# Optimization experiments

Hardware: AMD Instinct MI355X
Metric: run time of the kernel (lower is better)

The kernel has to match this reference:

```python
import jax, jax.numpy as jnp
import numpy as np


def setup_inputs() -> dict:
    key = jax.random.key(0)
    k1, k2, k3, k4, k5 = jax.random.split(key, 5)
    D, K, W, C = 2048, 4096, 4096, 1000
    deep_feats = jax.random.normal(k1, (1, D), dtype=jnp.float32)
    cls_score = jax.random.normal(k2, (K, C), dtype=jnp.float32)
    target = jax.random.randint(k3, (1,), 0, C, dtype=jnp.int64)
    n = jax.random.normal(k4, (K, D), dtype=jnp.float32)
    w = jax.random.uniform(k5, (W, K), dtype=jnp.float32)
    return {"deep_feats": deep_feats, "cls_score": cls_score, "target": target, "n": n, "w": w}


def reference(deep_feats, cls_score, target, n, w):
    # d[idx] = ||deep_feats[0] - n[idx]||_2, shape [K]
    diff = deep_feats[0][None, :] - n            # [K, D]
    d = jnp.sqrt(jnp.sum(diff * diff, axis=-1))  # [K]
    # rho[idy] = softmax_idx(-w[idy] * d), shape [W, K]
    rho = jax.nn.softmax(-w * d[None, :], axis=-1)
    # f_loss = sum_{idy,idx} w[idy,idx] * d[idx]
    f_loss = jnp.sum(w * d[None, :])
    # per-neighbor cross entropy: ce[idx] = -log_softmax(cls_score[idx])[target]
    logp = jax.nn.log_softmax(cls_score, axis=-1)  # [K, C]
    ce = -logp[:, target[0]]                        # [K]
    # g_loss = sum_{idy,idx} rho[idy,idx] * ce[idx]
    g_loss = jnp.sum(rho @ ce)
    return g_loss + f_loss
```

## Files before the change

### kernel.cpp

```cpp
#include <hip/hip_runtime.h>
#include <math.h>

constexpr int KN = 4096;
constexpr int DN = 2048;
constexpr int CN = 1000;
constexpr int WN = 4096;

__device__ __forceinline__ float waveSum(float v) {
#pragma unroll
    for (int o = 32; o > 0; o >>= 1) v += __shfl_xor(v, o, 64);
    return v;
}
__device__ __forceinline__ float waveMax(float v) {
#pragma unroll
    for (int o = 32; o > 0; o >>= 1) v = fmaxf(v, __shfl_xor(v, o, 64));
    return v;
}

constexpr int S1_DIST_BLOCKS = KN / 4;
constexpr int S1_CE_BLOCKS   = KN / 4;

__global__ __launch_bounds__(256) void stage1_kernel(
    const float* __restrict__ deep, const float* __restrict__ nmat,
    const float* __restrict__ cls, const int* __restrict__ target,
    float* __restrict__ d_arr, float* __restrict__ ce_arr,
    float* __restrict__ out)
{
    const int b    = blockIdx.x;
    const int tid  = threadIdx.x;
    const int wv   = tid >> 6;
    const int lane = tid & 63;

    if (b == 0 && tid == 0)
        __hip_atomic_store(out, 0.0f, __ATOMIC_RELAXED, __HIP_MEMORY_SCOPE_AGENT);

    if (b < S1_DIST_BLOCKS) {
        const int row = b * 4 + wv;
        const float4* nrow = (const float4*)(nmat + (size_t)row * DN);
        const float4* df   = (const float4*)deep;
        float acc = 0.f;
#pragma unroll
        for (int c = 0; c < 8; ++c) {
            const int i = lane + 64 * c;
            const float4 a = df[i];
            const float4 x = nrow[i];
            const float e0 = a.x - x.x, e1 = a.y - x.y, e2 = a.z - x.z, e3 = a.w - x.w;
            acc += e0 * e0 + e1 * e1 + e2 * e2 + e3 * e3;
        }
        acc = waveSum(acc);
        if (lane == 0) d_arr[row] = sqrtf(acc);
    } else {
        const int row = (b - S1_DIST_BLOCKS) * 4 + wv;
        const float4* x4 = (const float4*)(cls + (size_t)row * CN);
        float4 v[4];
#pragma unroll
        for (int j = 0; j < 4; ++j) {
            const int i = lane + 64 * j;
            v[j] = (i < CN / 4) ? x4[i]
                                : make_float4(-INFINITY, -INFINITY, -INFINITY, -INFINITY);
        }
        float mx = -INFINITY;
#pragma unroll
        for (int j = 0; j < 4; ++j)
            mx = fmaxf(mx, fmaxf(fmaxf(v[j].x, v[j].y), fmaxf(v[j].z, v[j].w)));
        const float m = waveMax(mx);
        float s = 0.f;
#pragma unroll
        for (int j = 0; j < 4; ++j)
            s += __expf(v[j].x - m) + __expf(v[j].y - m)
               + __expf(v[j].z - m) + __expf(v[j].w - m);
        s = waveSum(s);
        if (lane == 0)
            ce_arr[row] = m + __logf(s) - cls[(size_t)row * CN + target[0]];
    }
}

constexpr int S2_BLOCK_THREADS = 512;
constexpr int S2_ROWS_PER_BLK  = 8;
constexpr int S2_BLOCKS        = WN / S2_ROWS_PER_BLK;

__global__ __launch_bounds__(S2_BLOCK_THREADS) void stage2_kernel(
    const float* __restrict__ wmat, const float* __restrict__ d_arr,
    const float* __restrict__ ce_arr, float* __restrict__ out)
{
    __shared__ float4 sd[KN / 4];
    __shared__ float4 sc[KN / 4];
    __shared__ float  part[8];

    const int tid  = threadIdx.x;
    const int wv   = tid >> 6;
    const int lane = tid & 63;

    {
        const float4* d4 = (const float4*)d_arr;
        const float4* c4 = (const float4*)ce_arr;
#pragma unroll
        for (int j = 0; j < 2; ++j) {
            const int i = tid + S2_BLOCK_THREADS * j;
            sd[i] = d4[i];
            sc[i] = c4[i];
        }
    }
    __syncthreads();

    const int row = blockIdx.x * S2_ROWS_PER_BLK + wv;
    const float4* wrow = (const float4*)(wmat + (size_t)row * KN);

    float es = 0.f, ec = 0.f, fs = 0.f;
#pragma unroll
    for (int c = 0; c < 16; ++c) {
        const int i = lane + 64 * c;
        const float4 a  = wrow[i];
        const float4 dv = sd[i];
        const float4 cv = sc[i];
        float t, e;
        t = a.x * dv.x; fs += t; e = __expf(-t); es += e; ec += e * cv.x;
        t = a.y * dv.y; fs += t; e = __expf(-t); es += e; ec += e * cv.y;
        t = a.z * dv.z; fs += t; e = __expf(-t); es += e; ec += e * cv.z;
        t = a.w * dv.w; fs += t; e = __expf(-t); es += e; ec += e * cv.w;
    }
    es = waveSum(es);  ec = waveSum(ec);  fs = waveSum(fs);

    if (lane == 0) part[wv] = ec / es + fs;
    __syncthreads();
    if (tid == 0) {
        float acc = 0.f;
#pragma unroll
        for (int j = 0; j < 8; ++j) acc += part[j];
        atomicAdd(out, acc);
    }
}

extern "C" void kernel_launch(void* const* d_in, const int* in_sizes, int n_in,
                              void* d_out, int out_size, void* d_ws, size_t ws_size,
                              hipStream_t stream) {
    const float* deep   = (const float*)d_in[0];
    const float* cls    = (const float*)d_in[1];
    const int*   target = (const int*)d_in[2];
    const float* nmat   = (const float*)d_in[3];
    const float* wmat   = (const float*)d_in[4];

    float* ws     = (float*)d_ws;
    float* d_arr  = ws;
    float* ce_arr = ws + KN;
    float* out    = (float*)d_out;

    stage1_kernel<<<S1_DIST_BLOCKS + S1_CE_BLOCKS, 256, 0, stream>>>(
        deep, nmat, cls, target, d_arr, ce_arr, out);
    stage2_kernel<<<S2_BLOCKS, S2_BLOCK_THREADS, 0, stream>>>(
        wmat, d_arr, ce_arr, out);
}
```

Before: 29.50 us.

## Fuse both stages into one persistent kernel with a global grid barrier

Merges the distance/cross-entropy stage and the weighted softmax stage into a single kernel of 1024 blocks. Each block does one distance row and one CE row per wave, then waits at an atomic-counter grid barrier before computing four w rows. A last-block reduction writes the output deterministically instead of using atomicAdd. This removes one kernel launch boundary, but adds a memset, a spin barrier that relies on every block being co-resident, and each block now loads the full d/ce vectors into LDS.

After: 79.28 us. 2.69x slower.

```diff
diff --git a/kernel.cpp b/kernel.cpp
--- a/kernel.cpp
+++ b/kernel.cpp
@@ -5,6 +5,9 @@
 constexpr int DN = 2048;
 constexpr int CN = 1000;
 constexpr int WN = 4096;
+
+constexpr int NBLK = 1024;
+constexpr int NTHR = 256;
 
 __device__ __forceinline__ float waveSum(float v) {
 #pragma unroll
@@ -17,25 +20,26 @@
     return v;
 }
 
-constexpr int S1_DIST_BLOCKS = KN / 4;
-constexpr int S1_CE_BLOCKS   = KN / 4;
-
-__global__ __launch_bounds__(256) void stage1_kernel(
+__global__ __launch_bounds__(NTHR, 4) void fused_kernel(
     const float* __restrict__ deep, const float* __restrict__ nmat,
     const float* __restrict__ cls, const int* __restrict__ target,
+    const float* __restrict__ wmat,
     float* __restrict__ d_arr, float* __restrict__ ce_arr,
+    float* __restrict__ part, unsigned int* __restrict__ cnt,
     float* __restrict__ out)
 {
+    __shared__ float sd[KN];
+    __shared__ float sc[KN];
+    __shared__ float wpart[4];
+    __shared__ int   sLast;
+
     const int b    = blockIdx.x;
     const int tid  = threadIdx.x;
     const int wv   = tid >> 6;
     const int lane = tid & 63;
+    const int row  = b * 4 + wv;
 
-    if (b == 0 && tid == 0)
-        __hip_atomic_store(out, 0.0f, __ATOMIC_RELAXED, __HIP_MEMORY_SCOPE_AGENT);
-
-    if (b < S1_DIST_BLOCKS) {
-        const int row = b * 4 + wv;
+    {
         const float4* nrow = (const float4*)(nmat + (size_t)row * DN);
         const float4* df   = (const float4*)deep;
         float acc = 0.f;
@@ -48,9 +52,12 @@
             acc += e0 * e0 + e1 * e1 + e2 * e2 + e3 * e3;
         }
         acc = waveSum(acc);
-        if (lane == 0) d_arr[row] = sqrtf(acc);
-    } else {
-        const int row = (b - S1_DIST_BLOCKS) * 4 + wv;
+        if (lane == 0)
+            __hip_atomic_store(&d_arr[row], sqrtf(acc),
+                               __ATOMIC_RELAXED, __HIP_MEMORY_SCOPE_AGENT);
+    }
+
+    {
         const float4* x4 = (const float4*)(cls + (size_t)row * CN);
         float4 v[4];
 #pragma unroll
@@ -71,63 +78,71 @@
                + __expf(v[j].z - m) + __expf(v[j].w - m);
         s = waveSum(s);
         if (lane == 0)
-            ce_arr[row] = m + __logf(s) - cls[(size_t)row * CN + target[0]];
+            ce_arr[row] = 0.f,
+            __hip_atomic_store(&ce_arr[row], m + __logf(s) - cls[(size_t)row * CN + target[0]],
+                               __ATOMIC_RELAXED, __HIP_MEMORY_SCOPE_AGENT);
     }
-}
 
-constexpr int S2_BLOCK_THREADS = 512;
-constexpr int S2_ROWS_PER_BLK  = 8;
-constexpr int S2_BLOCKS        = WN / S2_ROWS_PER_BLK;
+    asm volatile("s_waitcnt vmcnt(0)");
+    __syncthreads();
 
-__global__ __launch_bounds__(S2_BLOCK_THREADS) void stage2_kernel(
-    const float* __restrict__ wmat, const float* __restrict__ d_arr,
-    const float* __restrict__ ce_arr, float* __restrict__ out)
-{
-    __shared__ float4 sd[KN / 4];
-    __shared__ float4 sc[KN / 4];
-    __shared__ float  part[8];
-
-    const int tid  = threadIdx.x;
-    const int wv   = tid >> 6;
-    const int lane = tid & 63;
-
-    {
-        const float4* d4 = (const float4*)d_arr;
-        const float4* c4 = (const float4*)ce_arr;
-#pragma unroll
-        for (int j = 0; j < 2; ++j) {
-            const int i = tid + S2_BLOCK_THREADS * j;
-            sd[i] = d4[i];
-            sc[i] = c4[i];
-        }
+    if (tid == 0) {
+        __hip_atomic_fetch_add(cnt, 1u, __ATOMIC_RELAXED, __HIP_MEMORY_SCOPE_AGENT);
+        while (__hip_atomic_load(cnt, __ATOMIC_RELAXED, __HIP_MEMORY_SCOPE_AGENT)
+               < (unsigned)NBLK)
+            __builtin_amdgcn_s_sleep(8);
     }
     __syncthreads();
 
-    const int row = blockIdx.x * S2_ROWS_PER_BLK + wv;
-    const float4* wrow = (const float4*)(wmat + (size_t)row * KN);
+#pragma unroll
+    for (int j = 0; j < 16; ++j) {
+        const int i = tid + NTHR * j;
+        sd[i] = __hip_atomic_load(&d_arr[i],  __ATOMIC_RELAXED, __HIP_MEMORY_SCOPE_AGENT);
+        sc[i] = __hip_atomic_load(&ce_arr[i], __ATOMIC_RELAXED, __HIP_MEMORY_SCOPE_AGENT);
+    }
+    __syncthreads();
 
-    float es = 0.f, ec = 0.f, fs = 0.f;
+    {
+        const float4* wrow = (const float4*)(wmat + (size_t)row * KN);
+        const float4* sd4  = (const float4*)sd;
+        const float4* sc4  = (const float4*)sc;
+        float es = 0.f, ec = 0.f, fs = 0.f;
 #pragma unroll
-    for (int c = 0; c < 16; ++c) {
-        const int i = lane + 64 * c;
-        const float4 a  = wrow[i];
-        const float4 dv = sd[i];
-        const float4 cv = sc[i];
-        float t, e;
-        t = a.x * dv.x; fs += t; e = __expf(-t); es += e; ec += e * cv.x;
-        t = a.y * dv.y; fs += t; e = __expf(-t); es += e; ec += e * cv.y;
-        t = a.z * dv.z; fs += t; e = __expf(-t); es += e; ec += e * cv.z;
-        t = a.w * dv.w; fs += t; e = __expf(-t); es += e; ec += e * cv.w;
+        for (int c = 0; c < 16; ++c) {
+            const int i = lane + 64 * c;
+            const float4 a  = wrow[i];
+            const float4 dv = sd4[i];
+            const float4 cv = sc4[i];
+            float t, e;
+            t = a.x * dv.x; fs += t; e = __expf(-t); es += e; ec += e * cv.x;
+            t = a.y * dv.y; fs += t; e = __expf(-t); es += e; ec += e * cv.y;
+            t = a.z * dv.z; fs += t; e = __expf(-t); es += e; ec += e * cv.z;
+            t = a.w * dv.w; fs += t; e = __expf(-t); es += e; ec += e * cv.w;
+        }
+        es = waveSum(es);  ec = waveSum(ec);  fs = waveSum(fs);
+        if (lane == 0) wpart[wv] = ec / es + fs;
     }
-    es = waveSum(es);  ec = waveSum(ec);  fs = waveSum(fs);
+    __syncthreads();
 
-    if (lane == 0) part[wv] = ec / es + fs;
+    if (tid == 0) {
+        const float psum = wpart[0] + wpart[1] + wpart[2] + wpart[3];
+        __hip_atomic_store(&part[b], psum, __ATOMIC_RELAXED, __HIP_MEMORY_SCOPE_AGENT);
+        asm volatile("s_waitcnt vmcnt(0)");
+        const unsigned prev = __hip_atomic_fetch_add(cnt + 1, 1u, __ATOMIC_RELAXED,
+                                                     __HIP_MEMORY_SCOPE_AGENT);
+        sLast = (prev == (unsigned)(NBLK - 1)) ? 1 : 0;
+    }
     __syncthreads();
-    if (tid == 0) {
+    if (sLast) {
         float acc = 0.f;
 #pragma unroll
-        for (int j = 0; j < 8; ++j) acc += part[j];
-        atomicAdd(out, acc);
+        for (int j = 0; j < 4; ++j)
+            acc += __hip_atomic_load(&part[tid + NTHR * j],
+                                     __ATOMIC_RELAXED, __HIP_MEMORY_SCOPE_AGENT);
+        acc = waveSum(acc);
+        if (lane == 0) wpart[wv] = acc;
+        __syncthreads();
+        if (tid == 0) out[0] = wpart[0] + wpart[1] + wpart[2] + wpart[3];
     }
 }
 
@@ -143,10 +158,11 @@
     float* ws     = (float*)d_ws;
     float* d_arr  = ws;
     float* ce_arr = ws + KN;
-    float* out    = (float*)d_out;
+    float* part   = ws + 2 * KN;
+    unsigned int* cnt = (unsigned int*)(ws + 2 * KN + NBLK);
 
-    stage1_kernel<<<S1_DIST_BLOCKS + S1_CE_BLOCKS, 256, 0, stream>>>(
-        deep, nmat, cls, target, d_arr, ce_arr, out);
-    stage2_kernel<<<S2_BLOCKS, S2_BLOCK_THREADS, 0, stream>>>(
-        wmat, d_arr, ce_arr, out);
+    hipMemsetAsync(cnt, 0, 2 * sizeof(unsigned int), stream);
+
+    fused_kernel<<<NBLK, NTHR, 0, stream>>>(
+        deep, nmat, cls, target, wmat, d_arr, ce_arr, part, cnt, (float*)d_out);
 }
```
